# Optimization experiments

Hardware: AMD Instinct MI355X
Metric: run time of the kernel (lower is better)

Reference implementation:

```python
import jax, jax.numpy as jnp
import numpy as np

NEG = -1e9  # masked_fill value


def _forward(input1, input2, wg1, wg2):
    S, E = input1.shape[0], wg1.shape[0]
    k = E // 4                      # expert_group_size
    num_2nd = E // 4
    capacity = int(2 * ((S + num_2nd - 1) // num_2nd))  # training-mode capacity, cf=1.0

    # --- first-level group gating ---
    group_logits = input1 @ wg1.T                     # [S,E]
    group_gates = jax.nn.softmax(group_logits.at[:, 0].set(NEG), axis=1)
    _, top_idx = jax.lax.top_k(group_gates, k)        # [S,k]
    rows = jnp.arange(S)[:, None]
    group_mask = jnp.zeros((S, E), dtype=bool).at[rows, top_idx].set(True)

    # --- second-level logits, masked to the selected group ---
    logits = input2 @ wg2.T                           # [S,E]
    gates = jax.nn.softmax(jnp.where(group_mask, logits, NEG), axis=1)

    # --- htop1gating ---
    indices1 = jnp.argmax(gates, axis=1)              # [S]
    mask1 = jax.nn.one_hot(indices1, E, dtype=jnp.int32)   # [S,E]
    gates1_s = (gates * mask1).sum(axis=1)            # [S]
    locations1 = jnp.cumsum(mask1, axis=0) - 1        # [S,E]

    me = jnp.mean(gates, axis=0)
    ce = jnp.mean(mask1.astype(gates.dtype), axis=0)
    l_aux = jnp.sum(me * ce) / num_2nd * (E * E)

    mask1 = mask1 * (locations1 < capacity).astype(mask1.dtype)
    locations1_s = jnp.sum(locations1 * mask1, axis=1)          # [S]
    gates1 = gates1_s[:, None] * mask1.astype(gates1_s.dtype)   # [S,E]
    locations1_sc = jax.nn.one_hot(locations1_s, capacity, dtype=gates1.dtype)  # [S,C]
    combine = gates1[:, :, None] * locations1_sc[:, None, :]    # [S,E,C]
    dispatch = combine.astype(bool)
    return l_aux, combine, dispatch


def setup_inputs() -> dict:
    key = jax.random.key(0)
    k1, k2, k3, k4 = jax.random.split(key, 4)
    S, D, E = 4096, 1024, 64
    return {
        "input1": jax.random.normal(k1, (S, D), dtype=jnp.float32),
        "input2": jax.random.normal(k2, (S, D), dtype=jnp.float32),
        "wg1": jax.random.normal(k3, (E, D), dtype=jnp.float32) * 0.02,
        "wg2": jax.random.normal(k4, (E, D), dtype=jnp.float32) * 0.02,
    }


def reference(input1, input2, wg1, wg2):
    return _forward(input1, input2, wg1, wg2)
```

## Files before the change

### kernel.cpp

```cpp
#include <hip/hip_runtime.h>
#include <cstdint>
#include <cstddef>

#define S_ROWS 4096
#define DIM 1024
#define NE 64
#define CAP 512
#define NEGV -1e9f

__global__ __launch_bounds__(256) void zerofill(float4* __restrict__ out4, long long n4,
                                                float* __restrict__ out, long long n) {
    long long i = (long long)blockIdx.x * blockDim.x + threadIdx.x;
    long long stride = (long long)gridDim.x * blockDim.x;
    float4 z; z.x = 0.f; z.y = 0.f; z.z = 0.f; z.w = 0.f;
    for (; i < n4; i += stride) out4[i] = z;
    if (blockIdx.x == 0 && threadIdx.x == 0) {
        for (long long j = n4 * 4; j < n; ++j) out[j] = 0.f;
    }
}

__global__ __launch_bounds__(256) void gemm64(const float* __restrict__ X1, const float* __restrict__ W1,
                                              const float* __restrict__ X2, const float* __restrict__ W2,
                                              float* __restrict__ L1, float* __restrict__ L2) {
    const float* __restrict__ X = blockIdx.y ? X2 : X1;
    const float* __restrict__ W = blockIdx.y ? W2 : W1;
    float* __restrict__ L = blockIdx.y ? L2 : L1;

    __shared__ float As[64][68];
    __shared__ float Bs[64][68];

    const int tid = threadIdx.x;
    const int row0 = blockIdx.x * 64;
    const int tx = tid & 15;
    const int ty = tid >> 4;

    float acc[4][4] = {};

    for (int kk = 0; kk < DIM; kk += 64) {
        __syncthreads();
        #pragma unroll
        for (int p = 0; p < 4; ++p) {
            int r  = (tid >> 4) + p * 16;
            int c4 = (tid & 15) * 4;
            float4 a = *(const float4*)&X[(size_t)(row0 + r) * DIM + kk + c4];
            *(float4*)&As[r][c4] = a;
            float4 w = *(const float4*)&W[(size_t)r * DIM + kk + c4];
            Bs[c4 + 0][r] = w.x;
            Bs[c4 + 1][r] = w.y;
            Bs[c4 + 2][r] = w.z;
            Bs[c4 + 3][r] = w.w;
        }
        __syncthreads();
        #pragma unroll
        for (int k4 = 0; k4 < 64; k4 += 4) {
            float4 a[4], b[4];
            #pragma unroll
            for (int i = 0; i < 4; ++i) a[i] = *(float4*)&As[ty * 4 + i][k4];
            #pragma unroll
            for (int t = 0; t < 4; ++t) b[t] = *(float4*)&Bs[k4 + t][tx * 4];
            #pragma unroll
            for (int i = 0; i < 4; ++i) {
                acc[i][0] += a[i].x * b[0].x + a[i].y * b[1].x + a[i].z * b[2].x + a[i].w * b[3].x;
                acc[i][1] += a[i].x * b[0].y + a[i].y * b[1].y + a[i].z * b[2].y + a[i].w * b[3].y;
                acc[i][2] += a[i].x * b[0].z + a[i].y * b[1].z + a[i].z * b[2].z + a[i].w * b[3].z;
                acc[i][3] += a[i].x * b[0].w + a[i].y * b[1].w + a[i].z * b[2].w + a[i].w * b[3].w;
            }
        }
    }
    #pragma unroll
    for (int i = 0; i < 4; ++i) {
        float4 v; v.x = acc[i][0]; v.y = acc[i][1]; v.z = acc[i][2]; v.w = acc[i][3];
        *(float4*)&L[(size_t)(row0 + ty * 4 + i) * NE + tx * 4] = v;
    }
}

__global__ __launch_bounds__(256) void gatek(const float* __restrict__ L1, const float* __restrict__ L2,
                                             float* __restrict__ gates, int* __restrict__ eidx,
                                             float* __restrict__ gval) {
    const int wid  = threadIdx.x >> 6;
    const int lane = threadIdx.x & 63;
    const int r = blockIdx.x * 4 + wid;

    float l1 = L1[(size_t)r * NE + lane];
    if (lane == 0) l1 = NEGV;

    int cnt = 0;
    #pragma unroll
    for (int j = 0; j < 64; ++j) {
        float vj = __shfl(l1, j);
        if (vj > l1 || (vj == l1 && j < lane)) ++cnt;
    }
    const bool sel = cnt < 16;

    float l2 = L2[(size_t)r * NE + lane];
    float ml = sel ? l2 : NEGV;

    float m = ml;
    #pragma unroll
    for (int o = 32; o; o >>= 1) m = fmaxf(m, __shfl_xor(m, o));
    float ex = expf(ml - m);
    float sum = ex;
    #pragma unroll
    for (int o = 32; o; o >>= 1) sum += __shfl_xor(sum, o);
    float g = ex / sum;

    gates[(size_t)r * NE + lane] = g;

    float bg = g; int bi = lane;
    #pragma unroll
    for (int o = 32; o; o >>= 1) {
        float og = __shfl_xor(bg, o);
        int   oi = __shfl_xor(bi, o);
        if (og > bg || (og == bg && oi < bi)) { bg = og; bi = oi; }
    }
    if (lane == 0) { eidx[r] = bi; gval[r] = bg; }
}

__global__ __launch_bounds__(256) void lauxk(const float* __restrict__ gates, const int* __restrict__ eidx,
                                             float* __restrict__ out) {
    const int e = blockIdx.x;
    float gs = 0.f; int cnt = 0;
    for (int s = threadIdx.x; s < S_ROWS; s += 256) {
        gs  += gates[(size_t)s * NE + e];
        cnt += (eidx[s] == e);
    }
    __shared__ float sg[4]; __shared__ int sc[4];
    #pragma unroll
    for (int o = 32; o; o >>= 1) { gs += __shfl_down(gs, o); cnt += __shfl_down(cnt, o); }
    const int wid = threadIdx.x >> 6, lane = threadIdx.x & 63;
    if (lane == 0) { sg[wid] = gs; sc[wid] = cnt; }
    __syncthreads();
    if (threadIdx.x == 0) {
        float G = sg[0] + sg[1] + sg[2] + sg[3];
        int   C = sc[0] + sc[1] + sc[2] + sc[3];
        atomicAdd(out, G * (float)C * (1.0f / 65536.0f));
    }
}

__global__ __launch_bounds__(256) void scatterk(const int* __restrict__ eidx, const float* __restrict__ gval,
                                                float* __restrict__ out) {
    const int s = blockIdx.x;
    const int my = eidx[s];
    int cnt = 0;
    for (int j = threadIdx.x; j < s; j += 256) cnt += (eidx[j] == my);
    __shared__ int sc[4];
    #pragma unroll
    for (int o = 32; o; o >>= 1) cnt += __shfl_down(cnt, o);
    const int wid = threadIdx.x >> 6, lane = threadIdx.x & 63;
    if (lane == 0) sc[wid] = cnt;
    __syncthreads();
    if (threadIdx.x == 0) {
        int rank = sc[0] + sc[1] + sc[2] + sc[3];
        if (rank < CAP) {
            size_t base = 1 + (((size_t)s * NE + my) * CAP + (size_t)rank);
            out[base] = gval[s];
            out[base + (size_t)S_ROWS * NE * CAP] = 1.0f;
        }
    }
}

extern "C" void kernel_launch(void* const* d_in, const int* in_sizes, int n_in,
                              void* d_out, int out_size, void* d_ws, size_t ws_size,
                              hipStream_t stream) {
    const float* in1 = (const float*)d_in[0];
    const float* in2 = (const float*)d_in[1];
    const float* wg1 = (const float*)d_in[2];
    const float* wg2 = (const float*)d_in[3];
    float* out = (float*)d_out;

    float* L1    = (float*)d_ws;
    float* L2    = L1 + (size_t)S_ROWS * NE;
    float* gates = L2 + (size_t)S_ROWS * NE;
    int*   eidx  = (int*)(gates + (size_t)S_ROWS * NE);
    float* gv    = (float*)(eidx + S_ROWS);

    long long n  = (long long)out_size;
    long long n4 = n >> 2;
    zerofill<<<2048, 256, 0, stream>>>((float4*)out, n4, out, n);

    dim3 g(64, 2);
    gemm64<<<g, 256, 0, stream>>>(in1, wg1, in2, wg2, L1, L2);
    gatek<<<S_ROWS / 4, 256, 0, stream>>>(L1, L2, gates, eidx, gv);
    lauxk<<<NE, 256, 0, stream>>>(gates, eidx, out);
    scatterk<<<S_ROWS, 256, 0, stream>>>(eidx, gv, out);
}
```

Measured before the change: 1.184 ms.

## Use nontemporal zero-fill, smaller GEMM tiles, and fuse aux-loss reduction into gating

The output zero-fill now uses nontemporal vector stores with twice the grid, to cut cache pollution on the very large output write. The logits GEMM moves to 32-row tiles so twice as many blocks run. The gating kernel processes four rows per wave and accumulates per-expert gate sums and argmax counts with shared-memory and global atomics. This removes the full gates buffer and the separate column-reduction kernel, at the cost of float atomics that make the sum order nondeterministic.

New measurement: 1.185 ms. No clear change (+0.1%).

```diff
diff --git a/kernel.cpp b/kernel.cpp
--- a/kernel.cpp
+++ b/kernel.cpp
@@ -8,12 +8,14 @@
 #define CAP 512
 #define NEGV -1e9f
 
-__global__ __launch_bounds__(256) void zerofill(float4* __restrict__ out4, long long n4,
+typedef float v4f __attribute__((ext_vector_type(4)));
+
+__global__ __launch_bounds__(256) void zerofill(v4f* __restrict__ out4, long long n4,
                                                 float* __restrict__ out, long long n) {
     long long i = (long long)blockIdx.x * blockDim.x + threadIdx.x;
     long long stride = (long long)gridDim.x * blockDim.x;
-    float4 z; z.x = 0.f; z.y = 0.f; z.z = 0.f; z.w = 0.f;
-    for (; i < n4; i += stride) out4[i] = z;
+    v4f z = {0.f, 0.f, 0.f, 0.f};
+    for (; i < n4; i += stride) __builtin_nontemporal_store(z, &out4[i]);
     if (blockIdx.x == 0 && threadIdx.x == 0) {
         for (long long j = n4 * 4; j < n; ++j) out[j] = 0.f;
     }
@@ -21,45 +23,55 @@
 
 __global__ __launch_bounds__(256) void gemm64(const float* __restrict__ X1, const float* __restrict__ W1,
                                               const float* __restrict__ X2, const float* __restrict__ W2,
-                                              float* __restrict__ L1, float* __restrict__ L2) {
+                                              float* __restrict__ L1, float* __restrict__ L2,
+                                              float* __restrict__ Gg, int* __restrict__ Cg) {
+    if (blockIdx.x == 0 && blockIdx.y == 0 && threadIdx.x < NE) {
+        Gg[threadIdx.x] = 0.f;
+        Cg[threadIdx.x] = 0;
+    }
     const float* __restrict__ X = blockIdx.y ? X2 : X1;
     const float* __restrict__ W = blockIdx.y ? W2 : W1;
     float* __restrict__ L = blockIdx.y ? L2 : L1;
 
-    __shared__ float As[64][68];
+    __shared__ float As[32][68];
     __shared__ float Bs[64][68];
 
     const int tid = threadIdx.x;
-    const int row0 = blockIdx.x * 64;
+    const int row0 = blockIdx.x * 32;
     const int tx = tid & 15;
     const int ty = tid >> 4;
 
-    float acc[4][4] = {};
+    float acc[2][4] = {};
 
     for (int kk = 0; kk < DIM; kk += 64) {
         __syncthreads();
         #pragma unroll
-        for (int p = 0; p < 4; ++p) {
+        for (int p = 0; p < 2; ++p) {
             int r  = (tid >> 4) + p * 16;
             int c4 = (tid & 15) * 4;
             float4 a = *(const float4*)&X[(size_t)(row0 + r) * DIM + kk + c4];
             *(float4*)&As[r][c4] = a;
-            float4 w = *(const float4*)&W[(size_t)r * DIM + kk + c4];
-            Bs[c4 + 0][r] = w.x;
-            Bs[c4 + 1][r] = w.y;
-            Bs[c4 + 2][r] = w.z;
-            Bs[c4 + 3][r] = w.w;
+        }
+        #pragma unroll
+        for (int p = 0; p < 4; ++p) {
+            int e  = (tid >> 4) + p * 16;
+            int c4 = (tid & 15) * 4;
+            float4 w = *(const float4*)&W[(size_t)e * DIM + kk + c4];
+            Bs[c4 + 0][e] = w.x;
+            Bs[c4 + 1][e] = w.y;
+            Bs[c4 + 2][e] = w.z;
+            Bs[c4 + 3][e] = w.w;
         }
         __syncthreads();
         #pragma unroll
         for (int k4 = 0; k4 < 64; k4 += 4) {
-            float4 a[4], b[4];
+            float4 a[2], b[4];
             #pragma unroll
-            for (int i = 0; i < 4; ++i) a[i] = *(float4*)&As[ty * 4 + i][k4];
+            for (int i = 0; i < 2; ++i) a[i] = *(float4*)&As[ty * 2 + i][k4];
             #pragma unroll
             for (int t = 0; t < 4; ++t) b[t] = *(float4*)&Bs[k4 + t][tx * 4];
             #pragma unroll
-            for (int i = 0; i < 4; ++i) {
+            for (int i = 0; i < 2; ++i) {
                 acc[i][0] += a[i].x * b[0].x + a[i].y * b[1].x + a[i].z * b[2].x + a[i].w * b[3].x;
                 acc[i][1] += a[i].x * b[0].y + a[i].y * b[1].y + a[i].z * b[2].y + a[i].w * b[3].y;
                 acc[i][2] += a[i].x * b[0].z + a[i].y * b[1].z + a[i].z * b[2].z + a[i].w * b[3].z;
@@ -68,73 +80,79 @@
         }
     }
     #pragma unroll
+    for (int i = 0; i < 2; ++i) {
+        float4 v; v.x = acc[i][0]; v.y = acc[i][1]; v.z = acc[i][2]; v.w = acc[i][3];
+        *(float4*)&L[(size_t)(row0 + ty * 2 + i) * NE + tx * 4] = v;
+    }
+}
+
+__global__ __launch_bounds__(256) void gatek2(const float* __restrict__ L1, const float* __restrict__ L2,
+                                              int* __restrict__ eidx, float* __restrict__ gval,
+                                              float* __restrict__ Gg, int* __restrict__ Cg) {
+    __shared__ float sG[4][NE];
+    __shared__ int hist[NE];
+    const int wid = threadIdx.x >> 6, lane = threadIdx.x & 63;
+    if (threadIdx.x < NE) hist[threadIdx.x] = 0;
+    __syncthreads();
+
+    const int r0 = blockIdx.x * 16 + wid * 4;
+    float gacc = 0.f;
+    #pragma unroll
     for (int i = 0; i < 4; ++i) {
-        float4 v; v.x = acc[i][0]; v.y = acc[i][1]; v.z = acc[i][2]; v.w = acc[i][3];
-        *(float4*)&L[(size_t)(row0 + ty * 4 + i) * NE + tx * 4] = v;
-    }
-}
-
-__global__ __launch_bounds__(256) void gatek(const float* __restrict__ L1, const float* __restrict__ L2,
-                                             float* __restrict__ gates, int* __restrict__ eidx,
-                                             float* __restrict__ gval) {
-    const int wid  = threadIdx.x >> 6;
-    const int lane = threadIdx.x & 63;
-    const int r = blockIdx.x * 4 + wid;
-
-    float l1 = L1[(size_t)r * NE + lane];
-    if (lane == 0) l1 = NEGV;
-
-    int cnt = 0;
-    #pragma unroll
-    for (int j = 0; j < 64; ++j) {
-        float vj = __shfl(l1, j);
-        if (vj > l1 || (vj == l1 && j < lane)) ++cnt;
-    }
-    const bool sel = cnt < 16;
-
-    float l2 = L2[(size_t)r * NE + lane];
-    float ml = sel ? l2 : NEGV;
-
-    float m = ml;
-    #pragma unroll
-    for (int o = 32; o; o >>= 1) m = fmaxf(m, __shfl_xor(m, o));
-    float ex = expf(ml - m);
-    float sum = ex;
-    #pragma unroll
-    for (int o = 32; o; o >>= 1) sum += __shfl_xor(sum, o);
-    float g = ex / sum;
-
-    gates[(size_t)r * NE + lane] = g;
-
-    float bg = g; int bi = lane;
-    #pragma unroll
-    for (int o = 32; o; o >>= 1) {
-        float og = __shfl_xor(bg, o);
-        int   oi = __shfl_xor(bi, o);
-        if (og > bg || (og == bg && oi < bi)) { bg = og; bi = oi; }
-    }
-    if (lane == 0) { eidx[r] = bi; gval[r] = bg; }
-}
-
-__global__ __launch_bounds__(256) void lauxk(const float* __restrict__ gates, const int* __restrict__ eidx,
-                                             float* __restrict__ out) {
-    const int e = blockIdx.x;
-    float gs = 0.f; int cnt = 0;
-    for (int s = threadIdx.x; s < S_ROWS; s += 256) {
-        gs  += gates[(size_t)s * NE + e];
-        cnt += (eidx[s] == e);
-    }
-    __shared__ float sg[4]; __shared__ int sc[4];
-    #pragma unroll
-    for (int o = 32; o; o >>= 1) { gs += __shfl_down(gs, o); cnt += __shfl_down(cnt, o); }
-    const int wid = threadIdx.x >> 6, lane = threadIdx.x & 63;
-    if (lane == 0) { sg[wid] = gs; sc[wid] = cnt; }
+        const int r = r0 + i;
+        float l1 = L1[(size_t)r * NE + lane];
+        if (lane == 0) l1 = NEGV;
+
+        int cnt = 0;
+        #pragma unroll
+        for (int j = 0; j < 64; ++j) {
+            float vj = __shfl(l1, j);
+            cnt += (vj > l1 || (vj == l1 && j < lane));
+        }
+        const bool sel = cnt < 16;
+
+        float l2 = L2[(size_t)r * NE + lane];
+        float ml = sel ? l2 : NEGV;
+
+        float m = ml;
+        #pragma unroll
+        for (int o = 32; o; o >>= 1) m = fmaxf(m, __shfl_xor(m, o));
+        float ex = expf(ml - m);
+        float sum = ex;
+        #pragma unroll
+        for (int o = 32; o; o >>= 1) sum += __shfl_xor(sum, o);
+        float g = ex / sum;
+        gacc += g;
+
+        float bg = g; int bi = lane;
+        #pragma unroll
+        for (int o = 32; o; o >>= 1) {
+            float og = __shfl_xor(bg, o);
+            int   oi = __shfl_xor(bi, o);
+            if (og > bg || (og == bg && oi < bi)) { bg = og; bi = oi; }
+        }
+        if (lane == 0) {
+            eidx[r] = bi;
+            gval[r] = bg;
+            atomicAdd(&hist[bi], 1);
+        }
+    }
+    sG[wid][lane] = gacc;
     __syncthreads();
-    if (threadIdx.x == 0) {
-        float G = sg[0] + sg[1] + sg[2] + sg[3];
-        int   C = sc[0] + sc[1] + sc[2] + sc[3];
-        atomicAdd(out, G * (float)C * (1.0f / 65536.0f));
-    }
+    if (threadIdx.x < NE) {
+        float g4 = sG[0][threadIdx.x] + sG[1][threadIdx.x] + sG[2][threadIdx.x] + sG[3][threadIdx.x];
+        atomicAdd(&Gg[threadIdx.x], g4);
+        atomicAdd(&Cg[threadIdx.x], hist[threadIdx.x]);
+    }
+}
+
+__global__ void lauxfin(const float* __restrict__ Gg, const int* __restrict__ Cg,
+                        float* __restrict__ out) {
+    const int lane = threadIdx.x;
+    float v = Gg[lane] * (float)Cg[lane];
+    #pragma unroll
+    for (int o = 32; o; o >>= 1) v += __shfl_xor(v, o);
+    if (lane == 0) out[0] = v * (1.0f / 65536.0f);
 }
 
 __global__ __launch_bounds__(256) void scatterk(const int* __restrict__ eidx, const float* __restrict__ gval,
@@ -168,19 +186,20 @@
     const float* wg2 = (const float*)d_in[3];
     float* out = (float*)d_out;
 
-    float* L1    = (float*)d_ws;
-    float* L2    = L1 + (size_t)S_ROWS * NE;
-    float* gates = L2 + (size_t)S_ROWS * NE;
-    int*   eidx  = (int*)(gates + (size_t)S_ROWS * NE);
-    float* gv    = (float*)(eidx + S_ROWS);
+    float* L1   = (float*)d_ws;
+    float* L2   = L1 + (size_t)S_ROWS * NE;
+    int*   eidx = (int*)(L2 + (size_t)S_ROWS * NE);
+    float* gv   = (float*)(eidx + S_ROWS);
+    float* Gg   = gv + S_ROWS;
+    int*   Cg   = (int*)(Gg + NE);
 
     long long n  = (long long)out_size;
     long long n4 = n >> 2;
-    zerofill<<<2048, 256, 0, stream>>>((float4*)out, n4, out, n);
-
-    dim3 g(64, 2);
-    gemm64<<<g, 256, 0, stream>>>(in1, wg1, in2, wg2, L1, L2);
-    gatek<<<S_ROWS / 4, 256, 0, stream>>>(L1, L2, gates, eidx, gv);
-    lauxk<<<NE, 256, 0, stream>>>(gates, eidx, out);
+    zerofill<<<4096, 256, 0, stream>>>((v4f*)out, n4, out, n);
+
+    dim3 g(128, 2);
+    gemm64<<<g, 256, 0, stream>>>(in1, wg1, in2, wg2, L1, L2, Gg, Cg);
+    gatek2<<<S_ROWS / 16, 256, 0, stream>>>(L1, L2, eidx, gv, Gg, Cg);
+    lauxfin<<<1, 64, 0, stream>>>(Gg, Cg, out);
     scatterk<<<S_ROWS, 256, 0, stream>>>(eidx, gv, out);
 }
```
